# Kernel optimization log

Hardware: AMD Instinct MI355X
Metric: run time of the kernel (lower is better)

The kernel has to match this reference:

```python
import jax, jax.numpy as jnp
import numpy as np
from math import sqrt


def setup_inputs() -> dict:
    key = jax.random.key(0)
    ks = jax.random.split(key, 5)
    B, S, D = 4, 2048, 1024
    scale = 0.02
    return {
        "x": jax.random.normal(ks[0], (B, S, D), dtype=jnp.float32),
        "Wq": jax.random.normal(ks[1], (D, D), dtype=jnp.float32) * scale,
        "Wk": jax.random.normal(ks[2], (D, D), dtype=jnp.float32) * scale,
        "Wv": jax.random.normal(ks[3], (D, D), dtype=jnp.float32) * scale,
        "Wo": jax.random.normal(ks[4], (D, D), dtype=jnp.float32) * scale,
    }


def reference(x, Wq, Wk, Wv, Wo):
    NUM_HEAD = 16
    B, S, D = x.shape
    d_k = D // NUM_HEAD

    # fused QKV projection: weights are (d_model, d_in), applied as W @ x^T -> x @ W^T
    q = jnp.einsum('od,bsd->bso', Wq, x)
    k = jnp.einsum('od,bsd->bso', Wk, x)
    v = jnp.einsum('od,bsd->bso', Wv, x)

    def split_heads(t):  # [B,S,D] -> [B,H,S,d_k]
        return t.reshape(B, S, NUM_HEAD, d_k).transpose(0, 2, 1, 3)

    q, k, v = split_heads(q), split_heads(k), split_heads(v)

    # naive causal attention: full [B,H,S,S] score matrix
    scores = jnp.einsum('bhqd,bhkd->bhqk', q, k) / sqrt(d_k)
    causal = jnp.tril(jnp.ones((S, S), dtype=bool))  # [S,S]
    scores = jnp.where(causal, scores, -jnp.inf)
    probs = jax.nn.softmax(scores, axis=-1)
    attn = jnp.einsum('bhqk,bhkd->bhqd', probs, v)

    # merge heads: [B,H,S,d_k] -> [B,S,D]
    attn = attn.transpose(0, 2, 1, 3).reshape(B, S, D)
    # output projection
    return jnp.einsum('om,bsm->bso', Wo, attn)
```

## Files before the change

kernel.cpp:

```cpp
#include <hip/hip_runtime.h>
#include <hip/hip_bf16.h>
#include <stdint.h>

typedef unsigned short u16;
typedef __attribute__((ext_vector_type(8))) short bf16x8;
typedef __attribute__((ext_vector_type(4))) float f32x4;
typedef __attribute__((ext_vector_type(16))) float f32x16;

#define AS1 __attribute__((address_space(1)))
#define AS3 __attribute__((address_space(3)))

__device__ __forceinline__ u16 f2bf(float f) {
  union { float f; uint32_t u; } v; v.f = f;
  uint32_t u = v.u;
  return (u16)((u + 0x7FFFu + ((u >> 16) & 1u)) >> 16);
}

__device__ __forceinline__ uint32_t cvtpk(float lo, float hi) {
  uint32_t d;
  asm("v_cvt_pk_bf16_f32 %0, %1, %2" : "=v"(d) : "v"(lo), "v"(hi));
  return d;
}

__global__ __launch_bounds__(256) void cvt_all_kernel(const float* __restrict__ x,
    const float* __restrict__ Wq, const float* __restrict__ Wk,
    const float* __restrict__ Wv, const float* __restrict__ Wo,
    u16* __restrict__ xb, u16* __restrict__ wqb, u16* __restrict__ wkb,
    u16* __restrict__ wvb, u16* __restrict__ wob) {
  const int bid = blockIdx.x;
  const float* s;
  u16* d;
  int i;
  if (bid < 8192) {
    s = x; d = xb; i = bid * 256 + threadIdx.x;
  } else {
    const int w = (bid - 8192) >> 10;
    i = ((bid - 8192) & 1023) * 256 + threadIdx.x;
    s = (w == 0) ? Wq : (w == 1) ? Wk : (w == 2) ? Wv : Wo;
    d = (w == 0) ? wqb : (w == 1) ? wkb : (w == 2) ? wvb : wob;
  }
  float4 v = reinterpret_cast<const float4*>(s)[i];
  uint2 o;
  o.x = cvtpk(v.x, v.y);
  o.y = cvtpk(v.z, v.w);
  reinterpret_cast<uint2*>(d)[i] = o;
}

#define QSCALE 0.18033688011112042f

#define GK 64

template <int MODE, int KC, typename OutT>
__device__ __forceinline__ void gemm128_body(u16* __restrict__ lds,
    const u16* __restrict__ A, const u16* __restrict__ Bm, OutT* __restrict__ C,
    int M, int N, int by, int bx, float oscale) {
  const int tid = threadIdx.x;
  const int lane = tid & 63;
  const int wave = tid >> 6;
  const int wm = wave >> 1, wn = wave & 1;
  const int l15 = lane & 15, lhi = lane >> 4;
  const int axor = (lane & 7) << 4;

  const int srow = tid >> 3;
  const int scol = (((tid & 7) ^ (srow & 7)) << 4);
  const size_t Kb = (size_t)KC * 2;
  const uint8_t* Ag = (const uint8_t*)A + (size_t)(by * 128 + srow) * Kb + scol;
  const uint8_t* Bg = (const uint8_t*)Bm + (size_t)(bx * 128 + srow) * Kb + scol;
  uint8_t* Lb = (uint8_t*)lds;

#define STG128(bufi, kt)                                                                  \
  do {                                                                                    \
    _Pragma("unroll") for (int c = 0; c < 4; ++c) {                                       \
      __builtin_amdgcn_global_load_lds(                                                   \
          (const AS1 uint32_t*)(Ag + (size_t)c * 32 * Kb + (size_t)(kt) * 128),           \
          (AS3 uint32_t*)(Lb + (bufi) * 32768 + c * 4096 + tid * 16), 16, 0, 0);          \
      __builtin_amdgcn_global_load_lds(                                                   \
          (const AS1 uint32_t*)(Bg + (size_t)c * 32 * Kb + (size_t)(kt) * 128),           \
          (AS3 uint32_t*)(Lb + (bufi) * 32768 + 16384 + c * 4096 + tid * 16), 16, 0, 0);  \
    }                                                                                     \
  } while (0)

  const f32x4 fzero = {0.f, 0.f, 0.f, 0.f};
  f32x4 acc[4][4];
#pragma unroll
  for (int m = 0; m < 4; ++m)
#pragma unroll
    for (int n = 0; n < 4; ++n) acc[m][n] = fzero;

  constexpr int NT = KC / GK;

  STG128(0, 0);
  __syncthreads();

#pragma unroll
  for (int t = 0; t < NT; ++t) {
    const int cur = t & 1;
    if (t + 1 < NT) STG128(cur ^ 1, t + 1);
    const uint8_t* Ab = Lb + cur * 32768;
    const uint8_t* Bb = Ab + 16384;
    bf16x8 aF[4][2], bF[4][2];
#pragma unroll
    for (int ff = 0; ff < 4; ++ff)
#pragma unroll
      for (int ks = 0; ks < 2; ++ks) {
        aF[ff][ks] = *reinterpret_cast<const bf16x8*>(
            Ab + (wm * 64 + ff * 16 + l15) * 128 + ((ks * 64 + lhi * 16) ^ axor));
        bF[ff][ks] = *reinterpret_cast<const bf16x8*>(
            Bb + (wn * 64 + ff * 16 + l15) * 128 + ((ks * 64 + lhi * 16) ^ axor));
      }
    __builtin_amdgcn_s_setprio(1);
#pragma unroll
    for (int mm = 0; mm < 4; ++mm)
#pragma unroll
      for (int nn = 0; nn < 4; ++nn)
#pragma unroll
        for (int ks = 0; ks < 2; ++ks)
          acc[mm][nn] = __builtin_amdgcn_mfma_f32_16x16x32_bf16(aF[mm][ks], bF[nn][ks],
                                                                acc[mm][nn], 0, 0, 0);
    __builtin_amdgcn_s_setprio(0);
    __syncthreads();
  }

#pragma unroll
  for (int mf = 0; mf < 4; ++mf)
#pragma unroll
    for (int nf = 0; nf < 4; ++nf) {
      const int row0 = by * 128 + wm * 64 + mf * 16 + lhi * 4;
      const int col = bx * 128 + wn * 64 + nf * 16 + l15;
      if constexpr (MODE == 2) {
        uint2 pk;
        pk.x = cvtpk(acc[mf][nf][0], acc[mf][nf][1]);
        pk.y = cvtpk(acc[mf][nf][2], acc[mf][nf][3]);
        *reinterpret_cast<uint2*>((u16*)C + (size_t)col * M + row0) = pk;
      } else if constexpr (MODE == 1) {
#pragma unroll
        for (int r = 0; r < 4; ++r)
          ((float*)C)[(size_t)(row0 + r) * N + col] = acc[mf][nf][r];
      } else {
#pragma unroll
        for (int r = 0; r < 4; ++r)
          ((u16*)C)[(size_t)(row0 + r) * N + col] = f2bf(acc[mf][nf][r] * oscale);
      }
    }
#undef STG128
}

__global__ __launch_bounds__(256, 2) void gemm_qkv_kernel(const u16* __restrict__ A,
    const u16* __restrict__ W0, const u16* __restrict__ W1, const u16* __restrict__ W2,
    u16* __restrict__ OQ, u16* __restrict__ OK, u16* __restrict__ OVT, int M, int N) {
  __shared__ u16 lds[2][2][128 * GK];
  const int id = blockIdx.x;
  const int xcd = id & 7;
  const int slot = id >> 3;
  const int bz = slot >> 6;
  const int r = slot & 63;
  const int byi = r >> 3, bx = r & 7;
  const int by = xcd + 8 * byi;
  if (bz == 0)      gemm128_body<0, 1024, u16>(&lds[0][0][0], A, W0, OQ,  M, N, by, bx, QSCALE);
  else if (bz == 1) gemm128_body<0, 1024, u16>(&lds[0][0][0], A, W1, OK,  M, N, by, bx, 1.f);
  else              gemm128_body<2, 1024, u16>(&lds[0][0][0], A, W2, OVT, M, N, by, bx, 1.f);
}

__global__ __launch_bounds__(256, 2) void gemm_out_kernel(const u16* __restrict__ A,
    const u16* __restrict__ Bm, float* __restrict__ C, int M, int N) {
  __shared__ u16 lds[2][2][128 * GK];
  const int id = blockIdx.x;
  const int xcd = id & 7;
  const int slot = id >> 3;
  const int byi = slot >> 3, bx = slot & 7;
  const int by = xcd + 8 * byi;
  gemm128_body<1, 1024, float>(&lds[0][0][0], A, Bm, C, M, N, by, bx, 1.f);
}

#define KVB 64

__device__ __forceinline__ void attn_tile(const u16* __restrict__ KB,
    const u16* __restrict__ VB, const bf16x8 (&qf)[4], f32x16 (&acc)[2],
    float& mrow, float& lrow, int kv, int qv, int qr, int l31, int lh) {
  f32x16 sc[2];
#pragma unroll
  for (int bb = 0; bb < 2; ++bb) {
#pragma unroll
    for (int r = 0; r < 16; ++r) sc[bb][r] = 0.f;
#pragma unroll
    for (int dc = 0; dc < 4; ++dc) {
      const bf16x8 kf = *reinterpret_cast<const bf16x8*>(
          KB + (bb * 32 + l31) * 64 + (((dc * 2 + lh) ^ (l31 & 7)) << 3));
      sc[bb] = __builtin_amdgcn_mfma_f32_32x32x16_bf16(kf, qf[dc], sc[bb], 0, 0, 0);
    }
  }

  const bool msk = (kv + KVB - 1 > qv);
  float bmax = -3e38f;
#pragma unroll
  for (int bb = 0; bb < 2; ++bb)
#pragma unroll
    for (int r = 0; r < 16; ++r) {
      float v = sc[bb][r];
      if (msk) {
        const int kvg = kv + bb * 32 + (r & 3) + 8 * (r >> 2) + 4 * lh;
        v = (kvg > qr) ? -1e30f : v;
        sc[bb][r] = v;
      }
      bmax = fmaxf(bmax, v);
    }
  bmax = fmaxf(bmax, __shfl_xor(bmax, 32, 64));

  if (!__all(bmax <= mrow + 6.f)) {
    const float mn = fmaxf(mrow, bmax);
    const float fac = __builtin_amdgcn_exp2f(mrow - mn);
    mrow = mn;
    lrow *= fac;
#pragma unroll
    for (int db = 0; db < 2; ++db)
#pragma unroll
      for (int r = 0; r < 16; ++r) acc[db][r] *= fac;
  }

  float rs = 0.f;
#pragma unroll
  for (int bb = 0; bb < 2; ++bb)
#pragma unroll
    for (int r = 0; r < 16; ++r) {
      const float p = __builtin_amdgcn_exp2f(sc[bb][r] - mrow);
      sc[bb][r] = p;
      rs += p;
    }
  lrow += rs;

#pragma unroll
  for (int cc = 0; cc < 4; ++cc) {
    const int bb = cc >> 1, c2 = cc & 1;
    uint32_t a0 = cvtpk(sc[bb][8 * c2 + 0], sc[bb][8 * c2 + 1]);
    uint32_t a1 = cvtpk(sc[bb][8 * c2 + 2], sc[bb][8 * c2 + 3]);
    uint32_t b0 = cvtpk(sc[bb][8 * c2 + 4], sc[bb][8 * c2 + 5]);
    uint32_t b1 = cvtpk(sc[bb][8 * c2 + 6], sc[bb][8 * c2 + 7]);
    asm("v_permlane32_swap_b32 %0, %1" : "+v"(a0), "+v"(b0));
    asm("v_permlane32_swap_b32 %0, %1" : "+v"(a1), "+v"(b1));
    union { uint32_t u[4]; bf16x8 v8; } pf;
    pf.u[0] = a0; pf.u[1] = a1; pf.u[2] = b0; pf.u[3] = b1;
#pragma unroll
    for (int db = 0; db < 2; ++db) {
      const bf16x8 vfg = *reinterpret_cast<const bf16x8*>(
          VB + (db * 32 + l31) * 64 + (((cc * 2 + lh) ^ (l31 & 7)) << 3));
      acc[db] = __builtin_amdgcn_mfma_f32_32x32x16_bf16(vfg, pf.v8, acc[db], 0, 0, 0);
    }
  }
}

__global__ __launch_bounds__(256, 2) void attn_kernel(const u16* __restrict__ Q,
    const u16* __restrict__ Kg, const u16* __restrict__ VTg, u16* __restrict__ O,
    int S, int H, int Dm, int T) {
  const int bh = blockIdx.x;
  const int b = bh / H, h = bh % H;
  const int y = blockIdx.y;
  const int qh0 = 1920 - 128 * y;
  const int ql0 = 128 * y;
  const int tid = threadIdx.x;
  const int lane = tid & 63, wave = tid >> 6;
  const int l31 = lane & 31, lh = lane >> 5;

  __shared__ u16 KVs[2][2][64 * 64];

  const u16* Qh = Q + ((size_t)b * S) * Dm + h * 64;
  const u16* Kh = Kg + ((size_t)b * S) * Dm + h * 64;
  const u16* Vh = VTg + (size_t)(h * 64) * T + (size_t)b * S;
  const int qvH = qh0 + wave * 32, qvL = ql0 + wave * 32;
  const int qrH = qvH + l31, qrL = qvL + l31;

  bf16x8 qfH[4], qfL[4];
#pragma unroll
  for (int dc = 0; dc < 4; ++dc) {
    qfH[dc] = *reinterpret_cast<const bf16x8*>(Qh + (size_t)qrH * Dm + dc * 16 + lh * 8);
    qfL[dc] = *reinterpret_cast<const bf16x8*>(Qh + (size_t)qrL * Dm + dc * 16 + lh * 8);
  }

  f32x16 accH[2], accL[2];
#pragma unroll
  for (int db = 0; db < 2; ++db)
#pragma unroll
    for (int r = 0; r < 16; ++r) { accH[db][r] = 0.f; accL[db][r] = 0.f; }
  float mH = -1e30f, lH = 0.f, mL = -1e30f, lL = 0.f;

#define STAGE(bufi, kvoff)                                                                     \
  do {                                                                                         \
    const int sr = tid >> 3;                                                                   \
    const int sc_ = (((tid & 7) ^ (sr & 7)) << 3);                                             \
    _Pragma("unroll") for (int j = 0; j < 2; ++j) {                                            \
      __builtin_amdgcn_global_load_lds(                                                        \
          (const AS1 uint32_t*)(Kh + (size_t)((kvoff) + j * 32 + sr) * Dm + sc_),              \
          (AS3 uint32_t*)(&KVs[bufi][0][j * 2048 + tid * 8]), 16, 0, 0);                       \
      __builtin_amdgcn_global_load_lds(                                                        \
          (const AS1 uint32_t*)(Vh + (size_t)(j * 32 + sr) * T + (kvoff) + sc_),               \
          (AS3 uint32_t*)(&KVs[bufi][1][j * 2048 + tid * 8]), 16, 0, 0);                       \
    }                                                                                          \
  } while (0)

  const int nt = (qh0 + 128) / 64;
  STAGE(0, 0);
  int buf = 0;

  for (int t = 0; t < nt; ++t) {
    __syncthreads();
    const int kv = t * KVB;
    if (t + 1 < nt) STAGE(buf ^ 1, (t + 1) * KVB);
    const u16* KB = KVs[buf][0];
    const u16* VB = KVs[buf][1];
    if (kv <= qvH + 31) attn_tile(KB, VB, qfH, accH, mH, lH, kv, qvH, qrH, l31, lh);
    if (kv <= qvL + 31) attn_tile(KB, VB, qfL, accL, mL, lL, kv, qvL, qrL, l31, lh);
    buf ^= 1;
  }

  lH += __shfl_xor(lH, 32, 64);
  lL += __shfl_xor(lL, 32, 64);
  const float invH = 1.f / lH, invL = 1.f / lL;
  __syncthreads();
  u16* Ost = &KVs[0][0][0];
  {
#pragma unroll
    for (int s = 0; s < 2; ++s) {
      const int row = s * 128 + wave * 32 + l31;
      const f32x16* ac = s ? accL : accH;
      const float inv = s ? invL : invH;
#pragma unroll
      for (int db = 0; db < 2; ++db)
#pragma unroll
        for (int g = 0; g < 4; ++g) {
          uint2 pk;
          pk.x = cvtpk(ac[db][4 * g + 0] * inv, ac[db][4 * g + 1] * inv);
          pk.y = cvtpk(ac[db][4 * g + 2] * inv, ac[db][4 * g + 3] * inv);
          const int blk = 4 * db + g;
          const int addr = row * 64 + (((blk ^ (row & 7)) << 3)) + 4 * lh;
          *reinterpret_cast<uint2*>(Ost + addr) = pk;
        }
    }
  }
  __syncthreads();
#pragma unroll
  for (int p = 0; p < 8; ++p) {
    const int idx = p * 256 + tid;
    const int row = idx >> 3, seg = idx & 7;
    const float4 v = *reinterpret_cast<const float4*>(Ost + row * 64 + ((seg ^ (row & 7)) << 3));
    const int q = (row < 128) ? (qh0 + row) : (ql0 + row - 128);
    *reinterpret_cast<float4*>(O + ((size_t)b * S + q) * Dm + h * 64 + seg * 8) = v;
  }
#undef STAGE
}

extern "C" void kernel_launch(void* const* d_in, const int* in_sizes, int n_in,
                              void* d_out, int out_size, void* d_ws, size_t ws_size,
                              hipStream_t stream) {
  const float* x  = (const float*)d_in[0];
  const float* Wq = (const float*)d_in[1];
  const float* Wk = (const float*)d_in[2];
  const float* Wv = (const float*)d_in[3];
  const float* Wo = (const float*)d_in[4];
  float* out = (float*)d_out;

  const int B = 4, S = 2048, D = 1024, H = 16;
  const int T = B * S;

  uint8_t* p = (uint8_t*)d_ws;
  u16* xb  = (u16*)p; p += (size_t)T * D * 2;
  u16* wqb = (u16*)p; p += (size_t)D * D * 2;
  u16* wkb = (u16*)p; p += (size_t)D * D * 2;
  u16* wvb = (u16*)p; p += (size_t)D * D * 2;
  u16* wob = (u16*)p; p += (size_t)D * D * 2;
  u16* Qb  = (u16*)p; p += (size_t)T * D * 2;
  u16* Kb  = (u16*)p; p += (size_t)T * D * 2;
  u16* VTb = (u16*)p; p += (size_t)D * T * 2;
  u16* Ab  = xb;

  cvt_all_kernel<<<dim3(12288), dim3(256), 0, stream>>>(x, Wq, Wk, Wv, Wo,
                                                        xb, wqb, wkb, wvb, wob);

  gemm_qkv_kernel<<<dim3(1536), dim3(256), 0, stream>>>(xb, wqb, wkb, wvb, Qb, Kb, VTb, T, D);

  attn_kernel<<<dim3(B * H, 8), dim3(256), 0, stream>>>(Qb, Kb, VTb, Ab, S, H, D, T);

  gemm_out_kernel<<<dim3(512), dim3(256), 0, stream>>>(Ab, wob, out, T, D);
}
```

Baseline: 145.3 us.

## Enlarge attention KV tile to 128 and process 32-key sub-blocks with per-block causal skip

Doubles the KV tile staged into LDS per iteration from 64 to 128 keys, which halves the number of barriers and pipeline stages. Each tile is processed as four 32-key sub-blocks with online softmax, so fully masked sub-blocks are skipped and masking is applied only on diagonal sub-blocks. Max and sum are now computed with tree reductions. The V layout and swizzle change to 128-wide rows. The cost is LDS use doubling to 64KB per block, which may reduce occupancy, and more frequent online-softmax rescale checks.

```diff
diff --git a/kernel.cpp b/kernel.cpp
--- a/kernel.cpp
+++ b/kernel.cpp
@@ -172,77 +172,66 @@
   gemm128_body<1, 1024, float>(&lds[0][0][0], A, Bm, C, M, N, by, bx, 1.f);
 }
 
-#define KVB 64
-
-__device__ __forceinline__ void attn_tile(const u16* __restrict__ KB,
+#define KVB 128
+
+__device__ __forceinline__ void attn_bb(const u16* __restrict__ KB,
     const u16* __restrict__ VB, const bf16x8 (&qf)[4], f32x16 (&acc)[2],
-    float& mrow, float& lrow, int kv, int qv, int qr, int l31, int lh) {
-  f32x16 sc[2];
-#pragma unroll
-  for (int bb = 0; bb < 2; ++bb) {
-#pragma unroll
-    for (int r = 0; r < 16; ++r) sc[bb][r] = 0.f;
-#pragma unroll
-    for (int dc = 0; dc < 4; ++dc) {
-      const bf16x8 kf = *reinterpret_cast<const bf16x8*>(
-          KB + (bb * 32 + l31) * 64 + (((dc * 2 + lh) ^ (l31 & 7)) << 3));
-      sc[bb] = __builtin_amdgcn_mfma_f32_32x32x16_bf16(kf, qf[dc], sc[bb], 0, 0, 0);
-    }
-  }
-
-  const bool msk = (kv + KVB - 1 > qv);
-  float bmax = -3e38f;
-#pragma unroll
-  for (int bb = 0; bb < 2; ++bb)
+    float& mrow, float& lrow, int kvb, int qr, bool boundary, int bb, int l31, int lh) {
+  f32x16 sc;
+#pragma unroll
+  for (int r = 0; r < 16; ++r) sc[r] = 0.f;
+#pragma unroll
+  for (int dc = 0; dc < 4; ++dc) {
+    const bf16x8 kf = *reinterpret_cast<const bf16x8*>(
+        KB + (bb * 32 + l31) * 64 + (((dc * 2 + lh) ^ (l31 & 7)) << 3));
+    sc = __builtin_amdgcn_mfma_f32_32x32x16_bf16(kf, qf[dc], sc, 0, 0, 0);
+  }
+  if (boundary) {
 #pragma unroll
     for (int r = 0; r < 16; ++r) {
-      float v = sc[bb][r];
-      if (msk) {
-        const int kvg = kv + bb * 32 + (r & 3) + 8 * (r >> 2) + 4 * lh;
-        v = (kvg > qr) ? -1e30f : v;
-        sc[bb][r] = v;
-      }
-      bmax = fmaxf(bmax, v);
-    }
+      const int kvg = kvb + (r & 3) + 8 * (r >> 2) + 4 * lh;
+      sc[r] = (kvg > qr) ? -1e30f : sc[r];
+    }
+  }
+  float t0 = fmaxf(sc[0], sc[8]),  t1 = fmaxf(sc[1], sc[9]);
+  float t2 = fmaxf(sc[2], sc[10]), t3 = fmaxf(sc[3], sc[11]);
+  float t4 = fmaxf(sc[4], sc[12]), t5 = fmaxf(sc[5], sc[13]);
+  float t6 = fmaxf(sc[6], sc[14]), t7 = fmaxf(sc[7], sc[15]);
+  t0 = fmaxf(t0, t4); t1 = fmaxf(t1, t5); t2 = fmaxf(t2, t6); t3 = fmaxf(t3, t7);
+  float bmax = fmaxf(fmaxf(t0, t1), fmaxf(t2, t3));
   bmax = fmaxf(bmax, __shfl_xor(bmax, 32, 64));
-
   if (!__all(bmax <= mrow + 6.f)) {
     const float mn = fmaxf(mrow, bmax);
     const float fac = __builtin_amdgcn_exp2f(mrow - mn);
     mrow = mn;
     lrow *= fac;
-#pragma unroll
-    for (int db = 0; db < 2; ++db)
-#pragma unroll
-      for (int r = 0; r < 16; ++r) acc[db][r] *= fac;
-  }
-
-  float rs = 0.f;
-#pragma unroll
-  for (int bb = 0; bb < 2; ++bb)
-#pragma unroll
-    for (int r = 0; r < 16; ++r) {
-      const float p = __builtin_amdgcn_exp2f(sc[bb][r] - mrow);
-      sc[bb][r] = p;
-      rs += p;
-    }
-  lrow += rs;
-
-#pragma unroll
-  for (int cc = 0; cc < 4; ++cc) {
-    const int bb = cc >> 1, c2 = cc & 1;
-    uint32_t a0 = cvtpk(sc[bb][8 * c2 + 0], sc[bb][8 * c2 + 1]);
-    uint32_t a1 = cvtpk(sc[bb][8 * c2 + 2], sc[bb][8 * c2 + 3]);
-    uint32_t b0 = cvtpk(sc[bb][8 * c2 + 4], sc[bb][8 * c2 + 5]);
-    uint32_t b1 = cvtpk(sc[bb][8 * c2 + 6], sc[bb][8 * c2 + 7]);
+    acc[0] *= fac;
+    acc[1] *= fac;
+  }
+#pragma unroll
+  for (int r = 0; r < 16; ++r) sc[r] = __builtin_amdgcn_exp2f(sc[r] - mrow);
+  float s0 = sc[0] + sc[8],  s1 = sc[1] + sc[9];
+  float s2 = sc[2] + sc[10], s3 = sc[3] + sc[11];
+  float s4 = sc[4] + sc[12], s5 = sc[5] + sc[13];
+  float s6 = sc[6] + sc[14], s7 = sc[7] + sc[15];
+  s0 += s4; s1 += s5; s2 += s6; s3 += s7;
+  lrow += (s0 + s1) + (s2 + s3);
+#pragma unroll
+  for (int cc = 0; cc < 2; ++cc) {
+    uint32_t a0 = cvtpk(sc[8 * cc + 0], sc[8 * cc + 1]);
+    uint32_t a1 = cvtpk(sc[8 * cc + 2], sc[8 * cc + 3]);
+    uint32_t b0 = cvtpk(sc[8 * cc + 4], sc[8 * cc + 5]);
+    uint32_t b1 = cvtpk(sc[8 * cc + 6], sc[8 * cc + 7]);
     asm("v_permlane32_swap_b32 %0, %1" : "+v"(a0), "+v"(b0));
     asm("v_permlane32_swap_b32 %0, %1" : "+v"(a1), "+v"(b1));
     union { uint32_t u[4]; bf16x8 v8; } pf;
     pf.u[0] = a0; pf.u[1] = a1; pf.u[2] = b0; pf.u[3] = b1;
+    const int c2 = bb * 2 + cc;
 #pragma unroll
     for (int db = 0; db < 2; ++db) {
+      const int blkv = ((c2 * 2 + lh) & 8) | (((c2 * 2 + lh) ^ (l31 & 7)) & 7);
       const bf16x8 vfg = *reinterpret_cast<const bf16x8*>(
-          VB + (db * 32 + l31) * 64 + (((cc * 2 + lh) ^ (l31 & 7)) << 3));
+          VB + (db * 32 + l31) * 128 + blkv * 8);
       acc[db] = __builtin_amdgcn_mfma_f32_32x32x16_bf16(vfg, pf.v8, acc[db], 0, 0, 0);
     }
   }
@@ -260,7 +249,7 @@
   const int lane = tid & 63, wave = tid >> 6;
   const int l31 = lane & 31, lh = lane >> 5;
 
-  __shared__ u16 KVs[2][2][64 * 64];
+  __shared__ u16 KVs[2][2][8192];
 
   const u16* Qh = Q + ((size_t)b * S) * Dm + h * 64;
   const u16* Kh = Kg + ((size_t)b * S) * Dm + h * 64;
@@ -284,19 +273,22 @@
 
 #define STAGE(bufi, kvoff)                                                                     \
   do {                                                                                         \
-    const int sr = tid >> 3;                                                                   \
-    const int sc_ = (((tid & 7) ^ (sr & 7)) << 3);                                             \
-    _Pragma("unroll") for (int j = 0; j < 2; ++j) {                                            \
+    const int rK = tid >> 3;                                                                   \
+    const int cK = (((tid & 7) ^ (rK & 7)) << 3);                                              \
+    const int rV = tid >> 4;                                                                   \
+    const int sV = tid & 15;                                                                   \
+    const int cV = (((sV & 8) | ((sV ^ (rV & 7)) & 7)) << 3);                                  \
+    _Pragma("unroll") for (int j = 0; j < 4; ++j) {                                            \
       __builtin_amdgcn_global_load_lds(                                                        \
-          (const AS1 uint32_t*)(Kh + (size_t)((kvoff) + j * 32 + sr) * Dm + sc_),              \
+          (const AS1 uint32_t*)(Kh + (size_t)((kvoff) + j * 32 + rK) * Dm + cK),               \
           (AS3 uint32_t*)(&KVs[bufi][0][j * 2048 + tid * 8]), 16, 0, 0);                       \
       __builtin_amdgcn_global_load_lds(                                                        \
-          (const AS1 uint32_t*)(Vh + (size_t)(j * 32 + sr) * T + (kvoff) + sc_),               \
+          (const AS1 uint32_t*)(Vh + (size_t)(j * 16 + rV) * T + (kvoff) + cV),                \
           (AS3 uint32_t*)(&KVs[bufi][1][j * 2048 + tid * 8]), 16, 0, 0);                       \
     }                                                                                          \
   } while (0)
 
-  const int nt = (qh0 + 128) / 64;
+  const int nt = 16 - y;
   STAGE(0, 0);
   int buf = 0;
 
@@ -306,8 +298,18 @@
     if (t + 1 < nt) STAGE(buf ^ 1, (t + 1) * KVB);
     const u16* KB = KVs[buf][0];
     const u16* VB = KVs[buf][1];
-    if (kv <= qvH + 31) attn_tile(KB, VB, qfH, accH, mH, lH, kv, qvH, qrH, l31, lh);
-    if (kv <= qvL + 31) attn_tile(KB, VB, qfL, accL, mL, lL, kv, qvL, qrL, l31, lh);
+#pragma unroll
+    for (int bb = 0; bb < 4; ++bb) {
+      const int kvb = kv + bb * 32;
+      if (kvb <= qvH + 31)
+        attn_bb(KB, VB, qfH, accH, mH, lH, kvb, qrH, (kvb + 31 > qvH), bb, l31, lh);
+    }
+#pragma unroll
+    for (int bb = 0; bb < 4; ++bb) {
+      const int kvb = kv + bb * 32;
+      if (kvb <= qvL + 31)
+        attn_bb(KB, VB, qfL, accL, mL, lL, kvb, qrL, (kvb + 31 > qvL), bb, l31, lh);
+    }
     buf ^= 1;
   }
 
```

Measured after the change: 136.7 us. 1.06x faster.
